# Optimization experiments

Measured on AMD Instinct MI355X. Metric: run time of the kernel, lower is better.

Reference implementation:

```python
import jax, jax.numpy as jnp
import numpy as np

N_NODES = 100000
N_EDGES = 1600000
D_IN = 480
D_OUT = 256
NEG_SLOPE = 0.2  # GATv2Conv default negative_slope


def setup_inputs() -> dict:
    key = jax.random.key(0)
    ks = jax.random.split(key, 8)
    s_in = 1.0 / np.sqrt(D_IN)
    s_out = 1.0 / np.sqrt(D_OUT)
    return {
        "x": jax.random.normal(ks[0], (N_NODES, D_IN), dtype=jnp.float32),
        "edge_index": jax.random.randint(ks[1], (2, N_EDGES), 0, N_NODES, dtype=jnp.int32),
        "W_l": jax.random.normal(ks[2], (D_IN, D_OUT), dtype=jnp.float32) * s_in,
        "b_l": jnp.zeros((D_OUT,), dtype=jnp.float32),
        "W_r": jax.random.normal(ks[3], (D_IN, D_OUT), dtype=jnp.float32) * s_in,
        "b_r": jnp.zeros((D_OUT,), dtype=jnp.float32),
        "att": jax.random.normal(ks[4], (D_OUT,), dtype=jnp.float32) * s_out,
        "bias": jnp.zeros((D_OUT,), dtype=jnp.float32),
    }


def reference(x, edge_index, W_l, b_l, W_r, b_r, att, bias):
    # Single GATv2Conv(480 -> 256, heads=1, concat=False), as built by
    # GAT(in=480, hidden=512, num_layers=1, out=256, v2=True, act='relu', norm=None)
    # (act is only applied between layers, so none here).
    src = edge_index[0]  # message source j
    dst = edge_index[1]  # aggregation target i

    x_l = x @ W_l + b_l  # [N, D_OUT] source-side transform
    x_r = x @ W_r + b_r  # [N, D_OUT] target-side transform

    # GATv2 attention logits: e_ij = att^T LeakyReLU(x_l[j] + x_r[i])
    h = x_l[src] + x_r[dst]                    # [E, D_OUT]
    h = jnp.where(h > 0, h, NEG_SLOPE * h)     # leaky_relu
    e = h @ att                                # [E]

    # segment softmax over incoming edges of each dst node (numerically stable)
    e_max = jax.ops.segment_max(e, dst, num_segments=N_NODES)
    e_max = jnp.where(jnp.isfinite(e_max), e_max, 0.0)  # nodes with no edges
    ex = jnp.exp(e - e_max[dst])                         # [E]
    denom = jax.ops.segment_sum(ex, dst, num_segments=N_NODES)
    alpha = ex / (denom[dst] + 1e-16)                    # PyG softmax eps

    # attention-weighted scatter-sum of source messages x_l[j]
    out = jax.ops.segment_sum(alpha[:, None] * x_l[src], dst, num_segments=N_NODES)
    return out + bias
```

## Files before the change

### kernel.cpp

```cpp
#include <hip/hip_runtime.h>
#include <hip/hip_bf16.h>

#define N_NODES 100000
#define N_EDGES 1600000
#define D_IN    480
#define D_OUT   256
#define NEG_SLOPE 0.2f
#define NKB     (D_IN / 32)

typedef __attribute__((ext_vector_type(8))) short bf16x8;
typedef __attribute__((ext_vector_type(4))) float f32x4;

__device__ __forceinline__ unsigned short f2bf_rn(float f) {
    unsigned u = __float_as_uint(f);
    return (unsigned short)((u + 0x7fffu + ((u >> 16) & 1u)) >> 16);
}

__device__ __forceinline__ void split_bf16(float f, unsigned short& h, unsigned short& l) {
    unsigned u  = __float_as_uint(f);
    unsigned hr = (u + 0x7fffu + ((u >> 16) & 1u)) >> 16;
    h = (unsigned short)hr;
    float fh = __uint_as_float(hr << 16);
    l = f2bf_rn(f - fh);
}

__global__ __launch_bounds__(256) void pack_w(
    const float* __restrict__ Wl, const float* __restrict__ Wr,
    unsigned short* __restrict__ whi, unsigned short* __restrict__ wlo)
{
    const int idx = blockIdx.x * 256 + threadIdx.x;
    if (idx >= D_IN * 512) return;
    const int k   = idx >> 9;
    const int col = idx & 511;
    const float f = (col < 256) ? Wl[(size_t)k * 256 + col]
                                : Wr[(size_t)k * 256 + (col - 256)];
    unsigned short h, l;
    split_bf16(f, h, l);
    const size_t o = ((size_t)((k >> 5) * 512 + col) << 5) | (size_t)(k & 31);
    whi[o] = h; wlo[o] = l;
}

__global__ __launch_bounds__(512) void gemm_mfma(
    const float* __restrict__ x,
    const unsigned short* __restrict__ whi,
    const unsigned short* __restrict__ wlo,
    const float* __restrict__ b_l, const float* __restrict__ b_r,
    float* __restrict__ yl, float* __restrict__ yr)
{
    __shared__ __align__(16) unsigned short Ahi[2][64 * 32];
    __shared__ __align__(16) unsigned short Alo[2][64 * 32];

    const int t    = threadIdx.x;
    const int wid  = t >> 6;
    const int lane = t & 63;
    const int r0   = blockIdx.x * 64;

    const int srow = t >> 3;
    const int sk4  = (t & 7) * 4;
    const int gr   = r0 + srow;
    const float* xrow   = x + (size_t)gr * D_IN;
    const bool  srow_ok = (gr < N_NODES);

    const int woff = srow * 32 + (((sk4 >> 3) ^ ((srow >> 1) & 3)) * 8) + (sk4 & 7);

    const int l15 = lane & 15;
    const int lg  = lane >> 4;

    int aoff[4];
    #pragma unroll
    for (int rf = 0; rf < 4; ++rf) {
        const int row = rf * 16 + l15;
        aoff[rf] = row * 32 + ((lg ^ ((row >> 1) & 3)) * 8);
    }

    f32x4 acc[4][4] = {};

    float4 xv = make_float4(0.f, 0.f, 0.f, 0.f);
    if (srow_ok) xv = *(const float4*)(xrow + sk4);

    for (int kb = 0; kb < NKB; ++kb) {
        const int p = kb & 1;
        {
            unsigned short h0,h1,h2,h3,l0,l1,l2,l3;
            split_bf16(xv.x, h0, l0); split_bf16(xv.y, h1, l1);
            split_bf16(xv.z, h2, l2); split_bf16(xv.w, h3, l3);
            *(uint2*)&Ahi[p][woff] = make_uint2((unsigned)h0 | ((unsigned)h1 << 16),
                                                (unsigned)h2 | ((unsigned)h3 << 16));
            *(uint2*)&Alo[p][woff] = make_uint2((unsigned)l0 | ((unsigned)l1 << 16),
                                                (unsigned)l2 | ((unsigned)l3 << 16));
        }
        float4 xv_next = make_float4(0.f, 0.f, 0.f, 0.f);
        if (kb + 1 < NKB && srow_ok)
            xv_next = *(const float4*)(xrow + (kb + 1) * 32 + sk4);

        __syncthreads();

        bf16x8 ah[4], al[4];
        #pragma unroll
        for (int rf = 0; rf < 4; ++rf) {
            ah[rf] = *(const bf16x8*)&Ahi[p][aoff[rf]];
            al[rf] = *(const bf16x8*)&Alo[p][aoff[rf]];
        }

        const size_t bbase = ((size_t)kb * 512 + wid * 64 + l15) * 32 + lg * 8;
        #pragma unroll
        for (int cf = 0; cf < 4; ++cf) {
            const size_t bo = bbase + (size_t)cf * 16 * 32;
            const bf16x8 bh = *(const bf16x8*)(whi + bo);
            const bf16x8 bl = *(const bf16x8*)(wlo + bo);
            #pragma unroll
            for (int rf = 0; rf < 4; ++rf) {
                acc[rf][cf] = __builtin_amdgcn_mfma_f32_16x16x32_bf16(ah[rf], bh, acc[rf][cf], 0, 0, 0);
                acc[rf][cf] = __builtin_amdgcn_mfma_f32_16x16x32_bf16(al[rf], bh, acc[rf][cf], 0, 0, 0);
                acc[rf][cf] = __builtin_amdgcn_mfma_f32_16x16x32_bf16(ah[rf], bl, acc[rf][cf], 0, 0, 0);
            }
        }
        xv = xv_next;
    }

    float* const y  = (wid < 4) ? yl : yr;
    const float* bp = (wid < 4) ? b_l : b_r;
    #pragma unroll
    for (int cf = 0; cf < 4; ++cf) {
        const int ocol  = (wid & 3) * 64 + cf * 16 + l15;
        const float bia = bp[ocol];
        #pragma unroll
        for (int rf = 0; rf < 4; ++rf) {
            const int row0 = r0 + rf * 16 + lg * 4;
            #pragma unroll
            for (int i = 0; i < 4; ++i) {
                if (row0 + i < N_NODES)
                    y[(size_t)(row0 + i) * D_OUT + ocol] = acc[rf][cf][i] + bia;
            }
        }
    }
}

__global__ void init_csr(unsigned* __restrict__ deg, unsigned* __restrict__ total)
{
    const int i = blockIdx.x * 256 + threadIdx.x;
    if (i < N_NODES) deg[i] = 0u;
    if (i == 0) *total = 0u;
}

__global__ void hist_k(const int* __restrict__ ei, unsigned* __restrict__ deg)
{
    const int e = blockIdx.x * 256 + threadIdx.x;
    if (e < N_EDGES) atomicAdd(&deg[ei[N_EDGES + e]], 1u);
}

__global__ void row_start_k(const unsigned* __restrict__ deg,
                            unsigned* __restrict__ row_start,
                            unsigned* __restrict__ cursor,
                            unsigned* __restrict__ total)
{
    const int i    = blockIdx.x * 256 + threadIdx.x;
    const int lane = threadIdx.x & 63;
    const unsigned d = (i < N_NODES) ? deg[i] : 0u;

    unsigned v = d;
    #pragma unroll
    for (int off = 1; off < 64; off <<= 1) {
        unsigned tt = __shfl_up(v, off, 64);
        if (lane >= off) v += tt;
    }
    const unsigned excl = v - d;
    const unsigned wave_total = __shfl(v, 63, 64);

    unsigned base = 0;
    if (lane == 0) base = atomicAdd(total, wave_total);
    base = __shfl(base, 0, 64);

    if (i < N_NODES) {
        row_start[i] = base + excl;
        cursor[i]    = base + excl;
    }
}

__global__ void scatter_k(const int* __restrict__ ei,
                          unsigned* __restrict__ cursor,
                          int* __restrict__ csr_src)
{
    const int e = blockIdx.x * 256 + threadIdx.x;
    if (e >= N_EDGES) return;
    const int dst = ei[N_EDGES + e];
    const unsigned pos = atomicAdd(&cursor[dst], 1u);
    csr_src[pos] = ei[e];
}

__global__ __launch_bounds__(256) void node_agg(
    const float* __restrict__ xl, const float* __restrict__ xr,
    const float* __restrict__ att, const int* __restrict__ csr_src,
    const unsigned* __restrict__ row_start, const unsigned* __restrict__ deg,
    const float* __restrict__ bias, float* __restrict__ out)
{
    const int node = (blockIdx.x * blockDim.x + threadIdx.x) >> 6;
    const int lane = threadIdx.x & 63;
    if (node >= N_NODES) return;

    const int start = (int)row_start[node];
    const int cnt   = (int)deg[node];
    const int end   = start + cnt;

    const float4 a  = *(const float4*)(att + lane * 4);
    const float4 r  = *(const float4*)(xr + (size_t)node * D_OUT + lane * 4);

    float  m = -INFINITY;
    float  s = 0.f;
    float4 acc = make_float4(0.f, 0.f, 0.f, 0.f);

    float4 l = make_float4(0.f, 0.f, 0.f, 0.f);
    if (start < end)
        l = *(const float4*)(xl + (size_t)csr_src[start] * D_OUT + lane * 4);

    for (int j = start; j < end; ++j) {
        float4 l_next = make_float4(0.f, 0.f, 0.f, 0.f);
        if (j + 1 < end)
            l_next = *(const float4*)(xl + (size_t)csr_src[j + 1] * D_OUT + lane * 4);

        float h0 = l.x + r.x, h1 = l.y + r.y, h2 = l.z + r.z, h3 = l.w + r.w;
        h0 = h0 > 0.f ? h0 : NEG_SLOPE * h0;
        h1 = h1 > 0.f ? h1 : NEG_SLOPE * h1;
        h2 = h2 > 0.f ? h2 : NEG_SLOPE * h2;
        h3 = h3 > 0.f ? h3 : NEG_SLOPE * h3;
        float e = h0 * a.x + h1 * a.y + h2 * a.z + h3 * a.w;
        #pragma unroll
        for (int off = 32; off > 0; off >>= 1)
            e += __shfl_xor(e, off, 64);

        const float m_new = fmaxf(m, e);
        const float scale = __expf(m - m_new);
        const float p     = __expf(e - m_new);
        s = s * scale + p;
        acc.x = acc.x * scale + p * l.x;
        acc.y = acc.y * scale + p * l.y;
        acc.z = acc.z * scale + p * l.z;
        acc.w = acc.w * scale + p * l.w;
        m = m_new;

        l = l_next;
    }

    const float inv = 1.f / (s + 1e-16f);
    const float4 bv = *(const float4*)(bias + lane * 4);
    float4 o;
    o.x = acc.x * inv + bv.x; o.y = acc.y * inv + bv.y;
    o.z = acc.z * inv + bv.z; o.w = acc.w * inv + bv.w;
    *(float4*)(out + (size_t)node * D_OUT + lane * 4) = o;
}

extern "C" void kernel_launch(void* const* d_in, const int* in_sizes, int n_in,
                              void* d_out, int out_size, void* d_ws, size_t ws_size,
                              hipStream_t stream)
{
    const float* x   = (const float*)d_in[0];
    const int*   ei  = (const int*)  d_in[1];
    const float* W_l = (const float*)d_in[2];
    const float* b_l = (const float*)d_in[3];
    const float* W_r = (const float*)d_in[4];
    const float* b_r = (const float*)d_in[5];
    const float* att = (const float*)d_in[6];
    const float* bias= (const float*)d_in[7];
    float* out = (float*)d_out;

    float*    xl        = (float*)d_ws;
    float*    xr        = xl + (size_t)N_NODES * D_OUT;
    int*      csr_src   = (int*)(xr + (size_t)N_NODES * D_OUT);
    unsigned* deg       = (unsigned*)(csr_src + N_EDGES);
    unsigned* row_start = deg + N_NODES;
    unsigned* cursor    = row_start + N_NODES;
    unsigned* total     = cursor + N_NODES;
    unsigned short* whi = (unsigned short*)(total + 64);
    unsigned short* wlo = whi + (size_t)NKB * 512 * 32;

    pack_w<<<(D_IN * 512 + 255) / 256, 256, 0, stream>>>(W_l, W_r, whi, wlo);

    gemm_mfma<<<(N_NODES + 63) / 64, 512, 0, stream>>>(
        x, whi, wlo, b_l, b_r, xl, xr);

    const int nb_nodes = (N_NODES + 255) / 256;
    const int nb_edges = (N_EDGES + 255) / 256;
    init_csr<<<nb_nodes, 256, 0, stream>>>(deg, total);
    hist_k<<<nb_edges, 256, 0, stream>>>(ei, deg);
    row_start_k<<<nb_nodes, 256, 0, stream>>>(deg, row_start, cursor, total);
    scatter_k<<<nb_edges, 256, 0, stream>>>(ei, cursor, csr_src);

    node_agg<<<(N_NODES + 3) / 4, 256, 0, stream>>>(
        xl, xr, att, csr_src, row_start, deg, bias, out);
}
```

Measured before the change: 1.036 ms.

## Restructure GEMM k-loop pipeline, unroll edge aggregation by two, memset CSR init

```diff
diff --git a/kernel.cpp b/kernel.cpp
--- a/kernel.cpp
+++ b/kernel.cpp
@@ -75,25 +75,31 @@
 
     f32x4 acc[4][4] = {};
 
-    float4 xv = make_float4(0.f, 0.f, 0.f, 0.f);
-    if (srow_ok) xv = *(const float4*)(xrow + sk4);
+    {
+        float4 xv = make_float4(0.f, 0.f, 0.f, 0.f);
+        if (srow_ok) xv = *(const float4*)(xrow + sk4);
+        unsigned short h0,h1,h2,h3,l0,l1,l2,l3;
+        split_bf16(xv.x, h0, l0); split_bf16(xv.y, h1, l1);
+        split_bf16(xv.z, h2, l2); split_bf16(xv.w, h3, l3);
+        *(uint2*)&Ahi[0][woff] = make_uint2((unsigned)h0 | ((unsigned)h1 << 16),
+                                            (unsigned)h2 | ((unsigned)h3 << 16));
+        *(uint2*)&Alo[0][woff] = make_uint2((unsigned)l0 | ((unsigned)l1 << 16),
+                                            (unsigned)l2 | ((unsigned)l3 << 16));
+    }
+    float4 xnext = make_float4(0.f, 0.f, 0.f, 0.f);
+    if (srow_ok) xnext = *(const float4*)(xrow + 32 + sk4);
+    __syncthreads();
 
     for (int kb = 0; kb < NKB; ++kb) {
         const int p = kb & 1;
-        {
-            unsigned short h0,h1,h2,h3,l0,l1,l2,l3;
-            split_bf16(xv.x, h0, l0); split_bf16(xv.y, h1, l1);
-            split_bf16(xv.z, h2, l2); split_bf16(xv.w, h3, l3);
-            *(uint2*)&Ahi[p][woff] = make_uint2((unsigned)h0 | ((unsigned)h1 << 16),
-                                                (unsigned)h2 | ((unsigned)h3 << 16));
-            *(uint2*)&Alo[p][woff] = make_uint2((unsigned)l0 | ((unsigned)l1 << 16),
-                                                (unsigned)l2 | ((unsigned)l3 << 16));
-        }
-        float4 xv_next = make_float4(0.f, 0.f, 0.f, 0.f);
-        if (kb + 1 < NKB && srow_ok)
-            xv_next = *(const float4*)(xrow + (kb + 1) * 32 + sk4);
-
-        __syncthreads();
+
+        const size_t bbase = ((size_t)kb * 512 + wid * 64 + l15) * 32 + lg * 8;
+        bf16x8 bh[4], bl[4];
+        #pragma unroll
+        for (int cf = 0; cf < 4; ++cf) {
+            bh[cf] = *(const bf16x8*)(whi + bbase + (size_t)cf * 512);
+            bl[cf] = *(const bf16x8*)(wlo + bbase + (size_t)cf * 512);
+        }
 
         bf16x8 ah[4], al[4];
         #pragma unroll
@@ -102,20 +108,40 @@
             al[rf] = *(const bf16x8*)&Alo[p][aoff[rf]];
         }
 
-        const size_t bbase = ((size_t)kb * 512 + wid * 64 + l15) * 32 + lg * 8;
-        #pragma unroll
-        for (int cf = 0; cf < 4; ++cf) {
-            const size_t bo = bbase + (size_t)cf * 16 * 32;
-            const bf16x8 bh = *(const bf16x8*)(whi + bo);
-            const bf16x8 bl = *(const bf16x8*)(wlo + bo);
+        if (kb + 1 < NKB) {
+            unsigned short h0,h1,h2,h3,l0,l1,l2,l3;
+            split_bf16(xnext.x, h0, l0); split_bf16(xnext.y, h1, l1);
+            split_bf16(xnext.z, h2, l2); split_bf16(xnext.w, h3, l3);
+            *(uint2*)&Ahi[p ^ 1][woff] = make_uint2((unsigned)h0 | ((unsigned)h1 << 16),
+                                                    (unsigned)h2 | ((unsigned)h3 << 16));
+            *(uint2*)&Alo[p ^ 1][woff] = make_uint2((unsigned)l0 | ((unsigned)l1 << 16),
+                                                    (unsigned)l2 | ((unsigned)l3 << 16));
+        }
+
+        float4 xn2 = make_float4(0.f, 0.f, 0.f, 0.f);
+        if (kb + 2 < NKB && srow_ok)
+            xn2 = *(const float4*)(xrow + (kb + 2) * 32 + sk4);
+
+        __builtin_amdgcn_s_setprio(1);
+        #pragma unroll
+        for (int cf = 0; cf < 4; ++cf)
             #pragma unroll
-            for (int rf = 0; rf < 4; ++rf) {
-                acc[rf][cf] = __builtin_amdgcn_mfma_f32_16x16x32_bf16(ah[rf], bh, acc[rf][cf], 0, 0, 0);
-                acc[rf][cf] = __builtin_amdgcn_mfma_f32_16x16x32_bf16(al[rf], bh, acc[rf][cf], 0, 0, 0);
-                acc[rf][cf] = __builtin_amdgcn_mfma_f32_16x16x32_bf16(ah[rf], bl, acc[rf][cf], 0, 0, 0);
-            }
-        }
-        xv = xv_next;
+            for (int rf = 0; rf < 4; ++rf)
+                acc[rf][cf] = __builtin_amdgcn_mfma_f32_16x16x32_bf16(ah[rf], bh[cf], acc[rf][cf], 0, 0, 0);
+        #pragma unroll
+        for (int cf = 0; cf < 4; ++cf)
+            #pragma unroll
+            for (int rf = 0; rf < 4; ++rf)
+                acc[rf][cf] = __builtin_amdgcn_mfma_f32_16x16x32_bf16(al[rf], bh[cf], acc[rf][cf], 0, 0, 0);
+        #pragma unroll
+        for (int cf = 0; cf < 4; ++cf)
+            #pragma unroll
+            for (int rf = 0; rf < 4; ++rf)
+                acc[rf][cf] = __builtin_amdgcn_mfma_f32_16x16x32_bf16(ah[rf], bl[cf], acc[rf][cf], 0, 0, 0);
+        __builtin_amdgcn_s_setprio(0);
+
+        __syncthreads();
+        xnext = xn2;
     }
 
     float* const y  = (wid < 4) ? yl : yr;
@@ -136,13 +162,6 @@
     }
 }
 
-__global__ void init_csr(unsigned* __restrict__ deg, unsigned* __restrict__ total)
-{
-    const int i = blockIdx.x * 256 + threadIdx.x;
-    if (i < N_NODES) deg[i] = 0u;
-    if (i == 0) *total = 0u;
-}
-
 __global__ void hist_k(const int* __restrict__ ei, unsigned* __restrict__ deg)
 {
     const int e = blockIdx.x * 256 + threadIdx.x;
@@ -209,36 +228,71 @@
     float  s = 0.f;
     float4 acc = make_float4(0.f, 0.f, 0.f, 0.f);
 
-    float4 l = make_float4(0.f, 0.f, 0.f, 0.f);
-    if (start < end)
-        l = *(const float4*)(xl + (size_t)csr_src[start] * D_OUT + lane * 4);
-
-    for (int j = start; j < end; ++j) {
-        float4 l_next = make_float4(0.f, 0.f, 0.f, 0.f);
-        if (j + 1 < end)
-            l_next = *(const float4*)(xl + (size_t)csr_src[j + 1] * D_OUT + lane * 4);
-
-        float h0 = l.x + r.x, h1 = l.y + r.y, h2 = l.z + r.z, h3 = l.w + r.w;
+    float4 lA = make_float4(0.f, 0.f, 0.f, 0.f);
+    float4 lB = make_float4(0.f, 0.f, 0.f, 0.f);
+    if (start     < end) lA = *(const float4*)(xl + (size_t)csr_src[start]     * D_OUT + lane * 4);
+    if (start + 1 < end) lB = *(const float4*)(xl + (size_t)csr_src[start + 1] * D_OUT + lane * 4);
+
+    int j = start;
+    for (; j + 1 < end; j += 2) {
+        float4 lC = make_float4(0.f, 0.f, 0.f, 0.f);
+        float4 lD = make_float4(0.f, 0.f, 0.f, 0.f);
+        if (j + 2 < end) lC = *(const float4*)(xl + (size_t)csr_src[j + 2] * D_OUT + lane * 4);
+        if (j + 3 < end) lD = *(const float4*)(xl + (size_t)csr_src[j + 3] * D_OUT + lane * 4);
+
+        float h0 = lA.x + r.x, h1 = lA.y + r.y, h2 = lA.z + r.z, h3 = lA.w + r.w;
         h0 = h0 > 0.f ? h0 : NEG_SLOPE * h0;
         h1 = h1 > 0.f ? h1 : NEG_SLOPE * h1;
         h2 = h2 > 0.f ? h2 : NEG_SLOPE * h2;
         h3 = h3 > 0.f ? h3 : NEG_SLOPE * h3;
-        float e = h0 * a.x + h1 * a.y + h2 * a.z + h3 * a.w;
+        float e0 = h0 * a.x + h1 * a.y + h2 * a.z + h3 * a.w;
+
+        float g0 = lB.x + r.x, g1 = lB.y + r.y, g2 = lB.z + r.z, g3 = lB.w + r.w;
+        g0 = g0 > 0.f ? g0 : NEG_SLOPE * g0;
+        g1 = g1 > 0.f ? g1 : NEG_SLOPE * g1;
+        g2 = g2 > 0.f ? g2 : NEG_SLOPE * g2;
+        g3 = g3 > 0.f ? g3 : NEG_SLOPE * g3;
+        float e1 = g0 * a.x + g1 * a.y + g2 * a.z + g3 * a.w;
+
+        #pragma unroll
+        for (int off = 32; off > 0; off >>= 1) {
+            e0 += __shfl_xor(e0, off, 64);
+            e1 += __shfl_xor(e1, off, 64);
+        }
+
+        const float m_new = fmaxf(fmaxf(m, e0), e1);
+        const float scale = __expf(m - m_new);
+        const float p0    = __expf(e0 - m_new);
+        const float p1    = __expf(e1 - m_new);
+        s = s * scale + p0 + p1;
+        acc.x = acc.x * scale + p0 * lA.x + p1 * lB.x;
+        acc.y = acc.y * scale + p0 * lA.y + p1 * lB.y;
+        acc.z = acc.z * scale + p0 * lA.z + p1 * lB.z;
+        acc.w = acc.w * scale + p0 * lA.w + p1 * lB.w;
+        m = m_new;
+
+        lA = lC; lB = lD;
+    }
+    if (j < end) {
+        float h0 = lA.x + r.x, h1 = lA.y + r.y, h2 = lA.z + r.z, h3 = lA.w + r.w;
+        h0 = h0 > 0.f ? h0 : NEG_SLOPE * h0;
+        h1 = h1 > 0.f ? h1 : NEG_SLOPE * h1;
+        h2 = h2 > 0.f ? h2 : NEG_SLOPE * h2;
+        h3 = h3 > 0.f ? h3 : NEG_SLOPE * h3;
+        float e0 = h0 * a.x + h1 * a.y + h2 * a.z + h3 * a.w;
         #pragma unroll
         for (int off = 32; off > 0; off >>= 1)
-            e += __shfl_xor(e, off, 64);
-
-        const float m_new = fmaxf(m, e);
+            e0 += __shfl_xor(e0, off, 64);
+
+        const float m_new = fmaxf(m, e0);
         const float scale = __expf(m - m_new);
-        const float p     = __expf(e - m_new);
-        s = s * scale + p;
-        acc.x = acc.x * scale + p * l.x;
-        acc.y = acc.y * scale + p * l.y;
-        acc.z = acc.z * scale + p * l.z;
-        acc.w = acc.w * scale + p * l.w;
+        const float p0    = __expf(e0 - m_new);
+        s = s * scale + p0;
+        acc.x = acc.x * scale + p0 * lA.x;
+        acc.y = acc.y * scale + p0 * lA.y;
+        acc.z = acc.z * scale + p0 * lA.z;
+        acc.w = acc.w * scale + p0 * lA.w;
         m = m_new;
-
-        l = l_next;
     }
 
     const float inv = 1.f / (s + 1e-16f);
@@ -267,10 +321,10 @@
     float*    xr        = xl + (size_t)N_NODES * D_OUT;
     int*      csr_src   = (int*)(xr + (size_t)N_NODES * D_OUT);
     unsigned* deg       = (unsigned*)(csr_src + N_EDGES);
-    unsigned* row_start = deg + N_NODES;
+    unsigned* total     = deg + N_NODES;
+    unsigned* row_start = total + 64;
     unsigned* cursor    = row_start + N_NODES;
-    unsigned* total     = cursor + N_NODES;
-    unsigned short* whi = (unsigned short*)(total + 64);
+    unsigned short* whi = (unsigned short*)(cursor + N_NODES);
     unsigned short* wlo = whi + (size_t)NKB * 512 * 32;
 
     pack_w<<<(D_IN * 512 + 255) / 256, 256, 0, stream>>>(W_l, W_r, whi, wlo);
@@ -278,9 +332,9 @@
     gemm_mfma<<<(N_NODES + 63) / 64, 512, 0, stream>>>(
         x, whi, wlo, b_l, b_r, xl, xr);
 
+    hipMemsetAsync(deg, 0, (size_t)(N_NODES + 1) * sizeof(unsigned), stream);
     const int nb_nodes = (N_NODES + 255) / 256;
     const int nb_edges = (N_EDGES + 255) / 256;
-    init_csr<<<nb_nodes, 256, 0, stream>>>(deg, total);
     hist_k<<<nb_edges, 256, 0, stream>>>(ei, deg);
     row_start_k<<<nb_nodes, 256, 0, stream>>>(deg, row_start, cursor, total);
     scatter_k<<<nb_edges, 256, 0, stream>>>(ei, cursor, csr_src);
```

After: 966.3 us. -6.7%, faster.
